# Performance work log

Measured on AMD Instinct MI355X. Metric: run time of the kernel, lower is better.

The kernel has to match this reference:

```python
import jax, jax.numpy as jnp
import numpy as np

CODEBOOK = 512


def setup_inputs() -> dict:
    key = jax.random.key(0)
    k1, k2 = jax.random.split(key)
    h = jax.random.normal(k1, (8, 128, 32, 32), dtype=jnp.float32)
    emb = jax.random.normal(k2, (CODEBOOK, 1), dtype=jnp.float32)
    return {"h": h, "emb": emb}


def reference(h, emb):
    # Scalar VQ: map each element of h to its nearest codebook entry
    # (embedding dim is 1, so distance is just |e - x|).
    flat = h.reshape(-1)                      # [N]
    codes = emb[:, 0]                         # [K]
    dist = jnp.abs(flat[:, None] - codes[None, :])   # [N, K]
    idx = jnp.argmin(dist, axis=1)            # [N]
    return codes[idx].reshape(h.shape)
```

## Files before the change

kernel.cpp:

```cpp
#include <hip/hip_runtime.h>

#define NCODE 512
#define NB 2048
#define NTHR 512

__global__ __launch_bounds__(NTHR) void quantize_fused(
        const float* __restrict__ emb,
        const float4* __restrict__ h4,
        float4* __restrict__ out4,
        int n4) {
    __shared__ __align__(16) unsigned long long s_tmp[NCODE];
    __shared__ float s_val[NCODE + 16];
    __shared__ unsigned short s_idx[NCODE + 16];
    __shared__ unsigned int s_excl[NB + 1];
    __shared__ unsigned short s_start[NB];
    __shared__ float s_red[16];
    __shared__ unsigned int s_wt[8];
    __shared__ int s_flag;

    const int t = threadIdx.x;
    const int lane = t & 63;
    const int wv = t >> 6;

    const float v = emb[t];

    float mn = v, mx = v;
    #pragma unroll
    for (int o = 32; o >= 1; o >>= 1) {
        mn = fminf(mn, __shfl_xor(mn, o));
        mx = fmaxf(mx, __shfl_xor(mx, o));
    }
    if (lane == 0) { s_red[wv] = mn; s_red[8 + wv] = mx; }
    if (t == 0) s_flag = 0;
    s_excl[t] = 0; s_excl[t + 512] = 0; s_excl[t + 1024] = 0; s_excl[t + 1536] = 0;
    if (t == 0) s_excl[NB] = 0;
    __syncthreads();

    float vmin, invw;
    {
        float m0 = s_red[0], M0 = s_red[8];
        #pragma unroll
        for (int i = 1; i < 8; ++i) { m0 = fminf(m0, s_red[i]); M0 = fmaxf(M0, s_red[8 + i]); }
        vmin = m0;
        float range = M0 - m0;
        invw = (range > 0.0f) ? ((float)NB / range) : 0.0f;
    }

    unsigned int fb = __float_as_uint(v);
    unsigned int u = fb ^ ((fb & 0x80000000u) ? 0xFFFFFFFFu : 0x80000000u);
    const unsigned long long myk = (((unsigned long long)u) << 16) | (unsigned int)t;

    int b;
    {
        float bf = fminf(fmaxf((v - vmin) * invw, 0.0f), (float)(NB - 1));
        b = (int)bf;
    }
    const unsigned int slot = atomicAdd(&s_excl[b], 1u);
    __syncthreads();

    unsigned int h0 = s_excl[4 * t], h1 = s_excl[4 * t + 1],
                 h2 = s_excl[4 * t + 2], h3 = s_excl[4 * t + 3];
    unsigned int s = h0 + h1 + h2 + h3;
    unsigned int incl = s;
    #pragma unroll
    for (int o = 1; o < 64; o <<= 1) {
        unsigned int w = __shfl_up(incl, o);
        if (lane >= o) incl += w;
    }
    if (lane == 63) s_wt[wv] = incl;
    __syncthreads();
    unsigned int base = 0;
    #pragma unroll
    for (int i = 0; i < 8; ++i) base += (i < wv) ? s_wt[i] : 0u;
    const unsigned int e0 = base + incl - s;
    const unsigned int c0 = e0, c1 = c0 + h0, c2 = c1 + h1, c3 = c2 + h2, c4 = c3 + h3;
    {
        int viol = 0, lo;
        lo = (int)c0 - 1; if (lo < 0) lo = 0; s_start[4 * t + 0] = (unsigned short)lo; viol |= ((int)c1 - 1 - lo) > 15;
        lo = (int)c1 - 1; if (lo < 0) lo = 0; s_start[4 * t + 1] = (unsigned short)lo; viol |= ((int)c2 - 1 - lo) > 15;
        lo = (int)c2 - 1; if (lo < 0) lo = 0; s_start[4 * t + 2] = (unsigned short)lo; viol |= ((int)c3 - 1 - lo) > 15;
        lo = (int)c3 - 1; if (lo < 0) lo = 0; s_start[4 * t + 3] = (unsigned short)lo; viol |= ((int)c4 - 1 - lo) > 15;
        if (viol) atomicOr(&s_flag, 1);
    }
    s_excl[4 * t] = c0; s_excl[4 * t + 1] = c1; s_excl[4 * t + 2] = c2; s_excl[4 * t + 3] = c3;
    if (t == NTHR - 1) s_excl[NB] = c4;
    __syncthreads();

    const unsigned int lo_b = s_excl[b];
    const unsigned int hi_b = s_excl[b + 1];
    s_tmp[lo_b + slot] = myk;
    __syncthreads();
    {
        int r = 0;
        unsigned int minEq = (unsigned int)t;
        for (unsigned int j = lo_b; j < hi_b; ++j) {
            unsigned long long k2 = s_tmp[j];
            r += (k2 < myk) ? 1 : 0;
            unsigned int u2 = (unsigned int)(k2 >> 16);
            unsigned int fb2 = u2 ^ ((u2 & 0x80000000u) ? 0x80000000u : 0xFFFFFFFFu);
            float v2 = __uint_as_float(fb2);
            if (v2 == v) {
                unsigned int i2 = (unsigned int)(k2 & 0xFFFFull);
                minEq = (i2 < minEq) ? i2 : minEq;
            }
        }
        const int pos = (int)lo_b + r;
        s_val[pos] = v;
        s_idx[pos] = (unsigned short)minEq;
    }
    if (t < 16) { s_val[NCODE + t] = __builtin_huge_valf(); s_idx[NCODE + t] = 0; }
    __syncthreads();

    const bool fallback = (s_flag != 0);

    const int gsize = gridDim.x * NTHR;
    for (int i = blockIdx.x * NTHR + t; i < n4; i += gsize) {
        float4 x4 = h4[i];
        float xs[4] = {x4.x, x4.y, x4.z, x4.w};
        float r[4];
        if (!fallback) {
            #pragma unroll
            for (int e = 0; e < 4; ++e) {
                float x = xs[e];
                float bfx = fminf(fmaxf((x - vmin) * invw, 0.0f), (float)(NB - 1));
                int pos = s_start[(int)bfx];
                float vc = s_val[pos];
                #pragma unroll
                for (int st = 8; st >= 1; st >>= 1) {
                    int np = pos + st;
                    float vn = s_val[np];
                    bool take = (vn <= x);
                    pos = take ? np : pos;
                    vc = take ? vn : vc;
                }
                int hi = pos + 1;
                float vh = s_val[hi];
                float dl = fabsf(x - vc), dh = fabsf(x - vh);
                bool ph = dh < dl;
                if (dh == dl) ph = (s_idx[hi] < s_idx[pos]);
                r[e] = ph ? vh : vc;
            }
        } else {
            #pragma unroll
            for (int e = 0; e < 4; ++e) {
                float x = xs[e];
                int pos = 0;
                float vc = s_val[0];
                #pragma unroll
                for (int st = NCODE / 2; st >= 1; st >>= 1) {
                    int np = pos + st;
                    float vn = s_val[np];
                    bool take = (vn <= x);
                    pos = take ? np : pos;
                    vc = take ? vn : vc;
                }
                int hi = pos + 1;
                float vh = s_val[hi];
                float dl = fabsf(x - vc), dh = fabsf(x - vh);
                bool ph = dh < dl;
                if (dh == dl) ph = (s_idx[hi] < s_idx[pos]);
                r[e] = ph ? vh : vc;
            }
        }
        out4[i] = make_float4(r[0], r[1], r[2], r[3]);
    }
}

extern "C" void kernel_launch(void* const* d_in, const int* in_sizes, int n_in,
                              void* d_out, int out_size, void* d_ws, size_t ws_size,
                              hipStream_t stream) {
    const float* h   = (const float*)d_in[0];
    const float* emb = (const float*)d_in[1];
    float* out = (float*)d_out;

    const int n = in_sizes[0];
    const int n4 = n / 4;
    const int blocks = 512;
    quantize_fused<<<blocks, NTHR, 0, stream>>>(
        emb, (const float4*)h, (float4*)out, n4);
}
```

Baseline: 12.32 us.

## Precompute exact decision thresholds into bucketed LUT and issue input loads early

After: 11.72 us (median of 2 runs). 4.9% less time.

```diff
diff --git a/kernel.cpp b/kernel.cpp
--- a/kernel.cpp
+++ b/kernel.cpp
@@ -1,168 +1,223 @@
 #include <hip/hip_runtime.h>
 
 #define NCODE 512
-#define NB 2048
-#define NTHR 512
+#define NB    2048
+#define NTHR  1024
+#define FINF  __builtin_huge_valf()
+
+__device__ __forceinline__ unsigned int fmap(float f) {
+    unsigned int b = __float_as_uint(f);
+    return b ^ ((b & 0x80000000u) ? 0xFFFFFFFFu : 0x80000000u);
+}
+__device__ __forceinline__ float funmap(unsigned int u) {
+    unsigned int b = (u & 0x80000000u) ? (u ^ 0x80000000u) : ~u;
+    return __uint_as_float(b);
+}
+__device__ __forceinline__ int bucket_of(float x, float vmin, float invw) {
+    float bf = fminf(fmaxf((x - vmin) * invw, 0.0f), (float)(NB - 1));
+    return (int)bf;
+}
+__device__ __forceinline__ bool pick_hi(float x, float vl, float vh,
+                                        unsigned int il, unsigned int ih) {
+    float dl = x - vl;
+    float dh = vh - x;
+    return (dh < dl) || ((dh == dl) && (ih < il));
+}
 
 __global__ __launch_bounds__(NTHR) void quantize_fused(
         const float* __restrict__ emb,
         const float4* __restrict__ h4,
         float4* __restrict__ out4,
         int n4) {
-    __shared__ __align__(16) unsigned long long s_tmp[NCODE];
+    __shared__ float4 s_lut[NB];
+    __shared__ unsigned int s_excl[NB + 1];
+    __shared__ unsigned long long s_tmp[NCODE];
     __shared__ float s_val[NCODE + 16];
-    __shared__ unsigned short s_idx[NCODE + 16];
-    __shared__ unsigned int s_excl[NB + 1];
-    __shared__ unsigned short s_start[NB];
-    __shared__ float s_red[16];
-    __shared__ unsigned int s_wt[8];
-    __shared__ int s_flag;
+    __shared__ float s_thr[NCODE];
+    __shared__ unsigned short s_idx[NCODE];
+    __shared__ float s_red[32];
+    __shared__ unsigned int s_wt[16];
 
     const int t = threadIdx.x;
     const int lane = t & 63;
     const int wv = t >> 6;
 
-    const float v = emb[t];
-
-    float mn = v, mx = v;
-    #pragma unroll
-    for (int o = 32; o >= 1; o >>= 1) {
-        mn = fminf(mn, __shfl_xor(mn, o));
-        mx = fmaxf(mx, __shfl_xor(mx, o));
-    }
-    if (lane == 0) { s_red[wv] = mn; s_red[8 + wv] = mx; }
-    if (t == 0) s_flag = 0;
-    s_excl[t] = 0; s_excl[t + 512] = 0; s_excl[t + 1024] = 0; s_excl[t + 1536] = 0;
+    const int gid = blockIdx.x * NTHR + t;
+    const bool live = (gid < n4);
+    float4 x4 = make_float4(0.f, 0.f, 0.f, 0.f);
+    if (live) x4 = h4[gid];
+
+    s_excl[t] = 0; s_excl[t + NTHR] = 0;
     if (t == 0) s_excl[NB] = 0;
+
+    float v = 0.0f;
+    if (t < NCODE) {
+        v = emb[t];
+        float mn = v, mx = v;
+        #pragma unroll
+        for (int o = 32; o >= 1; o >>= 1) {
+            mn = fminf(mn, __shfl_xor(mn, o));
+            mx = fmaxf(mx, __shfl_xor(mx, o));
+        }
+        if (lane == 0) { s_red[wv] = mn; s_red[16 + wv] = mx; }
+    }
     __syncthreads();
 
     float vmin, invw;
     {
-        float m0 = s_red[0], M0 = s_red[8];
-        #pragma unroll
-        for (int i = 1; i < 8; ++i) { m0 = fminf(m0, s_red[i]); M0 = fmaxf(M0, s_red[8 + i]); }
+        float m0 = s_red[0], M0 = s_red[16];
+        #pragma unroll
+        for (int i = 1; i < 8; ++i) { m0 = fminf(m0, s_red[i]); M0 = fmaxf(M0, s_red[16 + i]); }
         vmin = m0;
         float range = M0 - m0;
         invw = (range > 0.0f) ? ((float)NB / range) : 0.0f;
     }
 
-    unsigned int fb = __float_as_uint(v);
-    unsigned int u = fb ^ ((fb & 0x80000000u) ? 0xFFFFFFFFu : 0x80000000u);
-    const unsigned long long myk = (((unsigned long long)u) << 16) | (unsigned int)t;
-
-    int b;
+    int b = 0; unsigned int slot = 0;
+    unsigned long long myk = 0;
+    if (t < NCODE) {
+        myk = (((unsigned long long)fmap(v)) << 16) | (unsigned int)t;
+        b = bucket_of(v, vmin, invw);
+        slot = atomicAdd(&s_excl[b], 1u);
+    }
+    __syncthreads();
+
     {
-        float bf = fminf(fmaxf((v - vmin) * invw, 0.0f), (float)(NB - 1));
-        b = (int)bf;
-    }
-    const unsigned int slot = atomicAdd(&s_excl[b], 1u);
-    __syncthreads();
-
-    unsigned int h0 = s_excl[4 * t], h1 = s_excl[4 * t + 1],
-                 h2 = s_excl[4 * t + 2], h3 = s_excl[4 * t + 3];
-    unsigned int s = h0 + h1 + h2 + h3;
-    unsigned int incl = s;
-    #pragma unroll
-    for (int o = 1; o < 64; o <<= 1) {
-        unsigned int w = __shfl_up(incl, o);
-        if (lane >= o) incl += w;
-    }
-    if (lane == 63) s_wt[wv] = incl;
-    __syncthreads();
-    unsigned int base = 0;
-    #pragma unroll
-    for (int i = 0; i < 8; ++i) base += (i < wv) ? s_wt[i] : 0u;
-    const unsigned int e0 = base + incl - s;
-    const unsigned int c0 = e0, c1 = c0 + h0, c2 = c1 + h1, c3 = c2 + h2, c4 = c3 + h3;
-    {
-        int viol = 0, lo;
-        lo = (int)c0 - 1; if (lo < 0) lo = 0; s_start[4 * t + 0] = (unsigned short)lo; viol |= ((int)c1 - 1 - lo) > 15;
-        lo = (int)c1 - 1; if (lo < 0) lo = 0; s_start[4 * t + 1] = (unsigned short)lo; viol |= ((int)c2 - 1 - lo) > 15;
-        lo = (int)c2 - 1; if (lo < 0) lo = 0; s_start[4 * t + 2] = (unsigned short)lo; viol |= ((int)c3 - 1 - lo) > 15;
-        lo = (int)c3 - 1; if (lo < 0) lo = 0; s_start[4 * t + 3] = (unsigned short)lo; viol |= ((int)c4 - 1 - lo) > 15;
-        if (viol) atomicOr(&s_flag, 1);
-    }
-    s_excl[4 * t] = c0; s_excl[4 * t + 1] = c1; s_excl[4 * t + 2] = c2; s_excl[4 * t + 3] = c3;
-    if (t == NTHR - 1) s_excl[NB] = c4;
-    __syncthreads();
-
-    const unsigned int lo_b = s_excl[b];
-    const unsigned int hi_b = s_excl[b + 1];
-    s_tmp[lo_b + slot] = myk;
-    __syncthreads();
-    {
-        int r = 0;
-        unsigned int minEq = (unsigned int)t;
+        unsigned int h0 = s_excl[2 * t], h1 = s_excl[2 * t + 1];
+        unsigned int s = h0 + h1, incl = s;
+        #pragma unroll
+        for (int o = 1; o < 64; o <<= 1) {
+            unsigned int w = __shfl_up(incl, o);
+            if (lane >= o) incl += w;
+        }
+        if (lane == 63) s_wt[wv] = incl;
+        __syncthreads();
+        unsigned int base = 0;
+        #pragma unroll
+        for (int i = 0; i < 16; ++i) base += (i < wv) ? s_wt[i] : 0u;
+        unsigned int c0 = base + incl - s;
+        s_excl[2 * t] = c0; s_excl[2 * t + 1] = c0 + h0;
+        if (t == NTHR - 1) s_excl[NB] = c0 + h0 + h1;
+    }
+    __syncthreads();
+
+    unsigned int lo_b = 0, hi_b = 0;
+    if (t < NCODE) {
+        lo_b = s_excl[b]; hi_b = s_excl[b + 1];
+        s_tmp[lo_b + slot] = myk;
+    }
+    __syncthreads();
+
+    if (t < NCODE) {
+        int r = 0; unsigned int minEq = (unsigned int)t;
         for (unsigned int j = lo_b; j < hi_b; ++j) {
             unsigned long long k2 = s_tmp[j];
             r += (k2 < myk) ? 1 : 0;
-            unsigned int u2 = (unsigned int)(k2 >> 16);
-            unsigned int fb2 = u2 ^ ((u2 & 0x80000000u) ? 0x80000000u : 0xFFFFFFFFu);
-            float v2 = __uint_as_float(fb2);
+            float v2 = funmap((unsigned int)(k2 >> 16));
             if (v2 == v) {
                 unsigned int i2 = (unsigned int)(k2 & 0xFFFFull);
                 minEq = (i2 < minEq) ? i2 : minEq;
             }
         }
-        const int pos = (int)lo_b + r;
+        int pos = (int)lo_b + r;
         s_val[pos] = v;
         s_idx[pos] = (unsigned short)minEq;
-    }
-    if (t < 16) { s_val[NCODE + t] = __builtin_huge_valf(); s_idx[NCODE + t] = 0; }
-    __syncthreads();
-
-    const bool fallback = (s_flag != 0);
-
-    const int gsize = gridDim.x * NTHR;
-    for (int i = blockIdx.x * NTHR + t; i < n4; i += gsize) {
-        float4 x4 = h4[i];
+    } else if (t < NCODE + 16) {
+        s_val[t] = FINF;
+    }
+    __syncthreads();
+
+    float thrReg = FINF;
+    if (t < NCODE - 1) {
+        float vl = s_val[t], vh = s_val[t + 1];
+        unsigned int il = s_idx[t], ih = s_idx[t + 1];
+        if (vl == vh) {
+            thrReg = vl;
+        } else {
+            unsigned int ulo = fmap(vl), uhi = fmap(vh);
+            unsigned int um = fmap(0.5f * (vl + vh));
+            unsigned int a  = (um - ulo >= 8u) ? um - 8u : ulo;
+            unsigned int b2 = (uhi - um >= 8u) ? um + 8u : uhi;
+            if (!pick_hi(funmap(a),  vl, vh, il, ih)) ulo = a;
+            if ( pick_hi(funmap(b2), vl, vh, il, ih)) uhi = b2;
+            while (uhi - ulo > 1u) {
+                unsigned int mid = ulo + ((uhi - ulo) >> 1);
+                if (pick_hi(funmap(mid), vl, vh, il, ih)) uhi = mid; else ulo = mid;
+            }
+            thrReg = funmap(uhi);
+        }
+        s_thr[t] = thrReg;
+    } else if (t == NCODE - 1) {
+        s_thr[t] = FINF;
+    } else {
+        int t2 = t - NCODE;
+        s_excl[t2] = 0; s_excl[t2 + 512] = 0; s_excl[t2 + 1024] = 0; s_excl[t2 + 1536] = 0;
+        if (t2 == 0) s_excl[NB] = 0;
+    }
+    __syncthreads();
+
+    if (t < NCODE - 1) atomicAdd(&s_excl[bucket_of(thrReg, vmin, invw)], 1u);
+    __syncthreads();
+
+    {
+        unsigned int h0 = s_excl[2 * t], h1 = s_excl[2 * t + 1];
+        unsigned int s = h0 + h1, incl = s;
+        #pragma unroll
+        for (int o = 1; o < 64; o <<= 1) {
+            unsigned int w = __shfl_up(incl, o);
+            if (lane >= o) incl += w;
+        }
+        if (lane == 63) s_wt[wv] = incl;
+        __syncthreads();
+        unsigned int base = 0;
+        #pragma unroll
+        for (int i = 0; i < 16; ++i) base += (i < wv) ? s_wt[i] : 0u;
+        unsigned int c0 = base + incl - s;
+        s_excl[2 * t] = c0; s_excl[2 * t + 1] = c0 + h0;
+        if (t == NTHR - 1) s_excl[NB] = c0 + h0 + h1;
+    }
+    __syncthreads();
+
+    #pragma unroll
+    for (int k = 0; k < 2; ++k) {
+        int bb = 2 * t + k;
+        unsigned int j = s_excl[bb];
+        unsigned int cnt = s_excl[bb + 1] - j;
+        float4 w;
+        if (cnt <= 3u) {
+            w.x = (cnt >= 1u) ? s_thr[j]     : FINF;
+            w.y = (cnt >= 2u) ? s_thr[j + 1] : FINF;
+            w.z = (cnt >= 3u) ? s_thr[j + 2] : FINF;
+            w.w = __uint_as_float(j);
+        } else {
+            w.x = FINF; w.y = FINF; w.z = FINF;
+            w.w = __uint_as_float(j | 0x80000000u);
+        }
+        s_lut[bb] = w;
+    }
+    __syncthreads();
+
+    if (live) {
         float xs[4] = {x4.x, x4.y, x4.z, x4.w};
-        float r[4];
-        if (!fallback) {
-            #pragma unroll
-            for (int e = 0; e < 4; ++e) {
-                float x = xs[e];
-                float bfx = fminf(fmaxf((x - vmin) * invw, 0.0f), (float)(NB - 1));
-                int pos = s_start[(int)bfx];
-                float vc = s_val[pos];
+        float rr[4];
+        #pragma unroll
+        for (int e = 0; e < 4; ++e) {
+            float x = xs[e];
+            float4 L = s_lut[bucket_of(x, vmin, invw)];
+            unsigned int bits = __float_as_uint(L.w);
+            int r = (int)(bits & 0xFFFFu);
+            r += (x >= L.x) ? 1 : 0;
+            r += (x >= L.y) ? 1 : 0;
+            r += (x >= L.z) ? 1 : 0;
+            if (bits & 0x80000000u) {
+                r = 0;
                 #pragma unroll
-                for (int st = 8; st >= 1; st >>= 1) {
-                    int np = pos + st;
-                    float vn = s_val[np];
-                    bool take = (vn <= x);
-                    pos = take ? np : pos;
-                    vc = take ? vn : vc;
-                }
-                int hi = pos + 1;
-                float vh = s_val[hi];
-                float dl = fabsf(x - vc), dh = fabsf(x - vh);
-                bool ph = dh < dl;
-                if (dh == dl) ph = (s_idx[hi] < s_idx[pos]);
-                r[e] = ph ? vh : vc;
+                for (int st = 256; st >= 1; st >>= 1)
+                    r += (s_thr[r + st - 1] <= x) ? st : 0;
             }
-        } else {
-            #pragma unroll
-            for (int e = 0; e < 4; ++e) {
-                float x = xs[e];
-                int pos = 0;
-                float vc = s_val[0];
-                #pragma unroll
-                for (int st = NCODE / 2; st >= 1; st >>= 1) {
-                    int np = pos + st;
-                    float vn = s_val[np];
-                    bool take = (vn <= x);
-                    pos = take ? np : pos;
-                    vc = take ? vn : vc;
-                }
-                int hi = pos + 1;
-                float vh = s_val[hi];
-                float dl = fabsf(x - vc), dh = fabsf(x - vh);
-                bool ph = dh < dl;
-                if (dh == dl) ph = (s_idx[hi] < s_idx[pos]);
-                r[e] = ph ? vh : vc;
-            }
-        }
-        out4[i] = make_float4(r[0], r[1], r[2], r[3]);
+            rr[e] = s_val[r];
+        }
+        out4[gid] = make_float4(rr[0], rr[1], rr[2], rr[3]);
     }
 }
 
@@ -175,7 +230,7 @@
 
     const int n = in_sizes[0];
     const int n4 = n / 4;
-    const int blocks = 512;
+    const int blocks = (n4 + NTHR - 1) / NTHR;
     quantize_fused<<<blocks, NTHR, 0, stream>>>(
         emb, (const float4*)h, (float4*)out, n4);
 }
```
